# Kernel tuning notes

Measured on AMD Instinct MI355X. Metric: run time of the kernel, lower is better.

## Reference

```python
import jax, jax.numpy as jnp
import numpy as np

B, N, F = 32, 1024, 128
H = 256        # n_hidden and mlp_hidden widths
OUT = 3
BN_EPS = 1e-3  # keras BatchNormalization default epsilon


def setup_inputs() -> dict:
    key = jax.random.key(0)
    ks = jax.random.split(key, 16)
    x = jax.random.normal(ks[0], (B, N, F), dtype=jnp.float32)
    a = (jax.random.uniform(ks[1], (B, N, N)) < 0.02).astype(jnp.float32)
    eps = jnp.zeros((), dtype=jnp.float32)  # trainable GIN epsilon, init 0

    def dense_p(k, fi, fo):
        k1, k2 = jax.random.split(k)
        w = jax.random.normal(k1, (fi, fo), dtype=jnp.float32) * (1.0 / np.sqrt(fi))
        b = jnp.zeros((fo,), dtype=jnp.float32)
        return w, b

    def bn_p(k, f):
        k1, k2 = jax.random.split(k)
        g = 1.0 + 0.1 * jax.random.normal(k1, (f,), dtype=jnp.float32)
        be = 0.1 * jax.random.normal(k2, (f,), dtype=jnp.float32)
        m = 0.1 * jax.random.normal(jax.random.fold_in(k, 7), (f,), dtype=jnp.float32)
        v = jnp.ones((f,), dtype=jnp.float32)
        return g, be, m, v

    w1, b1 = dense_p(ks[2], F, H)
    g1, be1, m1, v1 = bn_p(ks[3], H)
    w2, b2 = dense_p(ks[4], H, H)
    g2, be2, m2, v2 = bn_p(ks[5], H)
    w3, b3 = dense_p(ks[6], H, H)   # final MLP dense -> n_hidden
    g3, be3, m3, v3 = bn_p(ks[7], H)
    wd, bd = dense_p(ks[8], H, OUT)
    return dict(x=x, a=a, eps=eps,
                w1=w1, b1=b1, g1=g1, be1=be1, m1=m1, v1=v1,
                w2=w2, b2=b2, g2=g2, be2=be2, m2=m2, v2=v2,
                w3=w3, b3=b3, g3=g3, be3=be3, m3=m3, v3=v3,
                wd=wd, bd=bd)


def _bn(h, g, be, m, v):
    # inference-mode batchnorm over last (feature) axis
    return (h - m) * (g / jnp.sqrt(v + BN_EPS)) + be


def reference(x, a, eps, w1, b1, g1, be1, m1, v1,
              w2, b2, g2, be2, m2, v2,
              w3, b3, g3, be3, m3, v3, wd, bd):
    # GIN aggregation: (1+eps)*x_i + sum_{j in N(i)} x_j
    agg = jnp.einsum('bij,bjf->bif', a, x)          # [B,N,F]
    h = (1.0 + eps) * x + agg
    # MLP: Dense->BN->relu x2 (mlp_hidden), then Dense(n_hidden)->BN->relu
    h = jax.nn.relu(_bn(h @ w1 + b1, g1, be1, m1, v1))  # [B,N,H]
    h = jax.nn.relu(_bn(h @ w2 + b2, g2, be2, m2, v2))
    h = jax.nn.relu(_bn(h @ w3 + b3, g3, be3, m3, v3))
    # global max pool over nodes, dropout(0) = identity, then head Dense(3)
    pooled = jnp.max(h, axis=1)                      # [B,H]
    return pooled @ wd + bd                          # [B,3]
```

## Files before the change

kernel.cpp:

```cpp
#include <hip/hip_runtime.h>

#define BN_EPS 1e-3f

typedef __attribute__((ext_vector_type(8))) short bf16x8;
typedef __attribute__((ext_vector_type(4))) float f32x4;

__device__ __forceinline__ short f2bf(float f) {
    union { float f; unsigned u; } a; a.f = f;
    unsigned r = a.u + 0x7fffu + ((a.u >> 16) & 1u);
    return (short)(r >> 16);
}
__device__ __forceinline__ float bf2f(short s) {
    union { unsigned u; float f; } a;
    a.u = ((unsigned)(unsigned short)s) << 16;
    return a.f;
}

__global__ __launch_bounds__(128) void agg_kernel(
    const float* __restrict__ x, const float* __restrict__ a,
    const float* __restrict__ epsp, float* __restrict__ h0) {
    const int row = blockIdx.x;
    const int b   = row >> 10;
    const int t   = threadIdx.x;

    __shared__ int idx[1024];
    __shared__ int cnt;
    if (t == 0) cnt = 0;
    __syncthreads();

    const float4* arow = reinterpret_cast<const float4*>(a + (size_t)row * 1024);
    float4 v0 = arow[t];
    float4 v1 = arow[t + 128];
    const int j0 = t * 4;
    if (v0.x != 0.f) idx[atomicAdd(&cnt, 1)] = j0 + 0;
    if (v0.y != 0.f) idx[atomicAdd(&cnt, 1)] = j0 + 1;
    if (v0.z != 0.f) idx[atomicAdd(&cnt, 1)] = j0 + 2;
    if (v0.w != 0.f) idx[atomicAdd(&cnt, 1)] = j0 + 3;
    if (v1.x != 0.f) idx[atomicAdd(&cnt, 1)] = 512 + j0 + 0;
    if (v1.y != 0.f) idx[atomicAdd(&cnt, 1)] = 512 + j0 + 1;
    if (v1.z != 0.f) idx[atomicAdd(&cnt, 1)] = 512 + j0 + 2;
    if (v1.w != 0.f) idx[atomicAdd(&cnt, 1)] = 512 + j0 + 3;
    __syncthreads();

    const int n = cnt;
    const float* xb = x + (size_t)b * (1024 * 128);
    float acc = (1.0f + epsp[0]) * xb[(size_t)(row & 1023) * 128 + t];
    for (int q = 0; q < n; ++q) {
        acc += xb[(size_t)idx[q] * 128 + t];
    }
    h0[(size_t)row * 128 + t] = acc;
}

__global__ __launch_bounds__(256) void prep_w(
    const float* __restrict__ w1, const float* __restrict__ w2,
    const float* __restrict__ w3, ushort* __restrict__ Wp) {
    const int k = blockIdx.x;
    const int c = threadIdx.x;
    const float* src; int kl, base;
    if (k < 128)      { src = w1; kl = k;       base = 0; }
    else if (k < 384) { src = w2; kl = k - 128; base = 65536; }
    else              { src = w3; kl = k - 384; base = 196608; }
    const float val = src[(size_t)kl * 256 + c];
    const short hi = f2bf(val);
    const short lo = f2bf(val - bf2f(hi));
    const int off = base + (kl >> 5) * 16384 + ((((kl >> 3) & 3) * 256 + c) * 8) + (kl & 7);
    Wp[off]        = (ushort)hi;
    Wp[off + 8192] = (ushort)lo;
}

__global__ __launch_bounds__(512, 2) void fused_mlp(
    const float* __restrict__ h0, const ushort* __restrict__ Wp,
    const float* __restrict__ b1, const float* __restrict__ g1,
    const float* __restrict__ be1, const float* __restrict__ m1,
    const float* __restrict__ v1,
    const float* __restrict__ b2, const float* __restrict__ g2,
    const float* __restrict__ be2, const float* __restrict__ m2,
    const float* __restrict__ v2,
    const float* __restrict__ b3, const float* __restrict__ g3,
    const float* __restrict__ be3, const float* __restrict__ m3,
    const float* __restrict__ v3,
    float* __restrict__ pool) {
    __shared__ __align__(16) ushort Wb[2][4][256][8];
    __shared__ __align__(16) ushort Ab[2][4][4][32][8];

    const int tid  = threadIdx.x;
    const int lane = tid & 63;
    const int wid  = tid >> 6;
    const int wr   = wid >> 1;
    const int wn   = wid & 1;
    const int lr   = lane & 15;
    const int kg   = lane >> 4;
    const int row0 = blockIdx.x * 128;

    f32x4 acc1[2][8] = {};
    f32x4 acc2[2][8] = {};

    const int arow = tid >> 2;
    const int akq  = tid & 3;
    const float* aptr = h0 + (size_t)(row0 + arow) * 128 + akq * 8;

    #pragma unroll
    for (int kc = 0; kc < 4; ++kc) {
        f32x4 a0 = *reinterpret_cast<const f32x4*>(aptr + kc * 32);
        f32x4 a1 = *reinterpret_cast<const f32x4*>(aptr + kc * 32 + 4);
        const f32x4* wsrc = reinterpret_cast<const f32x4*>(Wp + kc * 16384);
        f32x4 wv0 = wsrc[tid], wv1 = wsrc[512 + tid];
        f32x4 wv2 = wsrc[1024 + tid], wv3 = wsrc[1536 + tid];
        __syncthreads();
        {
            float av[8] = {a0.x, a0.y, a0.z, a0.w, a1.x, a1.y, a1.z, a1.w};
            bf16x8 hi, lo;
            #pragma unroll
            for (int e = 0; e < 8; ++e) {
                const short h = f2bf(av[e]);
                hi[e] = h; lo[e] = f2bf(av[e] - bf2f(h));
            }
            *reinterpret_cast<bf16x8*>(&Ab[0][arow >> 5][akq][arow & 31][0]) = hi;
            *reinterpret_cast<bf16x8*>(&Ab[1][arow >> 5][akq][arow & 31][0]) = lo;
        }
        f32x4* wdst = reinterpret_cast<f32x4*>(Wb);
        wdst[tid] = wv0; wdst[512 + tid] = wv1;
        wdst[1024 + tid] = wv2; wdst[1536 + tid] = wv3;
        __syncthreads();

        bf16x8 ah0 = *reinterpret_cast<bf16x8*>(&Ab[0][wr][kg][lr][0]);
        bf16x8 al0 = *reinterpret_cast<bf16x8*>(&Ab[1][wr][kg][lr][0]);
        bf16x8 ah1 = *reinterpret_cast<bf16x8*>(&Ab[0][wr][kg][16 + lr][0]);
        bf16x8 al1 = *reinterpret_cast<bf16x8*>(&Ab[1][wr][kg][16 + lr][0]);
        #pragma unroll
        for (int ni = 0; ni < 8; ++ni) {
            bf16x8 bh = *reinterpret_cast<bf16x8*>(&Wb[0][kg][wn * 128 + ni * 16 + lr][0]);
            bf16x8 bl = *reinterpret_cast<bf16x8*>(&Wb[1][kg][wn * 128 + ni * 16 + lr][0]);
            acc1[0][ni] = __builtin_amdgcn_mfma_f32_16x16x32_bf16(ah0, bh, acc1[0][ni], 0, 0, 0);
            acc1[0][ni] = __builtin_amdgcn_mfma_f32_16x16x32_bf16(ah0, bl, acc1[0][ni], 0, 0, 0);
            acc1[0][ni] = __builtin_amdgcn_mfma_f32_16x16x32_bf16(al0, bh, acc1[0][ni], 0, 0, 0);
            acc1[1][ni] = __builtin_amdgcn_mfma_f32_16x16x32_bf16(ah1, bh, acc1[1][ni], 0, 0, 0);
            acc1[1][ni] = __builtin_amdgcn_mfma_f32_16x16x32_bf16(ah1, bl, acc1[1][ni], 0, 0, 0);
            acc1[1][ni] = __builtin_amdgcn_mfma_f32_16x16x32_bf16(al1, bh, acc1[1][ni], 0, 0, 0);
        }
    }

    #pragma unroll
    for (int ni = 0; ni < 8; ++ni) {
        const int c = wn * 128 + ni * 16 + lr;
        const float s  = g1[c] * rsqrtf(v1[c] + BN_EPS);
        const float tt = be1[c] - m1[c] * s;
        const float bb = b1[c];
        #pragma unroll
        for (int mi = 0; mi < 2; ++mi)
            #pragma unroll
            for (int r = 0; r < 4; ++r)
                acc1[mi][ni][r] = fmaxf(fmaf(acc1[mi][ni][r] + bb, s, tt), 0.f);
    }

    #pragma unroll
    for (int kc = 0; kc < 8; ++kc) {
        const f32x4* wsrc = reinterpret_cast<const f32x4*>(Wp + 65536 + kc * 16384);
        f32x4 wv0 = wsrc[tid], wv1 = wsrc[512 + tid];
        f32x4 wv2 = wsrc[1024 + tid], wv3 = wsrc[1536 + tid];
        __syncthreads();
        if (wn == (kc >> 2)) {
            #pragma unroll
            for (int j = 0; j < 2; ++j) {
                const int ni  = (kc & 3) * 2 + j;
                const int kgw = j * 2 + (lr >> 3);
                const int e   = lr & 7;
                #pragma unroll
                for (int mi = 0; mi < 2; ++mi)
                    #pragma unroll
                    for (int r = 0; r < 4; ++r) {
                        const float val = acc1[mi][ni][r];
                        const short h = f2bf(val);
                        Ab[0][wr][kgw][mi * 16 + kg * 4 + r][e] = (ushort)h;
                        Ab[1][wr][kgw][mi * 16 + kg * 4 + r][e] = (ushort)f2bf(val - bf2f(h));
                    }
            }
        }
        f32x4* wdst = reinterpret_cast<f32x4*>(Wb);
        wdst[tid] = wv0; wdst[512 + tid] = wv1;
        wdst[1024 + tid] = wv2; wdst[1536 + tid] = wv3;
        __syncthreads();

        bf16x8 ah0 = *reinterpret_cast<bf16x8*>(&Ab[0][wr][kg][lr][0]);
        bf16x8 al0 = *reinterpret_cast<bf16x8*>(&Ab[1][wr][kg][lr][0]);
        bf16x8 ah1 = *reinterpret_cast<bf16x8*>(&Ab[0][wr][kg][16 + lr][0]);
        bf16x8 al1 = *reinterpret_cast<bf16x8*>(&Ab[1][wr][kg][16 + lr][0]);
        #pragma unroll
        for (int ni = 0; ni < 8; ++ni) {
            bf16x8 bh = *reinterpret_cast<bf16x8*>(&Wb[0][kg][wn * 128 + ni * 16 + lr][0]);
            bf16x8 bl = *reinterpret_cast<bf16x8*>(&Wb[1][kg][wn * 128 + ni * 16 + lr][0]);
            acc2[0][ni] = __builtin_amdgcn_mfma_f32_16x16x32_bf16(ah0, bh, acc2[0][ni], 0, 0, 0);
            acc2[0][ni] = __builtin_amdgcn_mfma_f32_16x16x32_bf16(ah0, bl, acc2[0][ni], 0, 0, 0);
            acc2[0][ni] = __builtin_amdgcn_mfma_f32_16x16x32_bf16(al0, bh, acc2[0][ni], 0, 0, 0);
            acc2[1][ni] = __builtin_amdgcn_mfma_f32_16x16x32_bf16(ah1, bh, acc2[1][ni], 0, 0, 0);
            acc2[1][ni] = __builtin_amdgcn_mfma_f32_16x16x32_bf16(ah1, bl, acc2[1][ni], 0, 0, 0);
            acc2[1][ni] = __builtin_amdgcn_mfma_f32_16x16x32_bf16(al1, bh, acc2[1][ni], 0, 0, 0);
        }
    }

    #pragma unroll
    for (int ni = 0; ni < 8; ++ni) {
        const int c = wn * 128 + ni * 16 + lr;
        const float s  = g2[c] * rsqrtf(v2[c] + BN_EPS);
        const float tt = be2[c] - m2[c] * s;
        const float bb = b2[c];
        #pragma unroll
        for (int mi = 0; mi < 2; ++mi)
            #pragma unroll
            for (int r = 0; r < 4; ++r)
                acc2[mi][ni][r] = fmaxf(fmaf(acc2[mi][ni][r] + bb, s, tt), 0.f);
    }

    #pragma unroll
    for (int mi = 0; mi < 2; ++mi)
        #pragma unroll
        for (int ni = 0; ni < 8; ++ni)
            #pragma unroll
            for (int r = 0; r < 4; ++r)
                acc1[mi][ni][r] = 0.f;

    #pragma unroll
    for (int kc = 0; kc < 8; ++kc) {
        const f32x4* wsrc = reinterpret_cast<const f32x4*>(Wp + 196608 + kc * 16384);
        f32x4 wv0 = wsrc[tid], wv1 = wsrc[512 + tid];
        f32x4 wv2 = wsrc[1024 + tid], wv3 = wsrc[1536 + tid];
        __syncthreads();
        if (wn == (kc >> 2)) {
            #pragma unroll
            for (int j = 0; j < 2; ++j) {
                const int ni  = (kc & 3) * 2 + j;
                const int kgw = j * 2 + (lr >> 3);
                const int e   = lr & 7;
                #pragma unroll
                for (int mi = 0; mi < 2; ++mi)
                    #pragma unroll
                    for (int r = 0; r < 4; ++r) {
                        const float val = acc2[mi][ni][r];
                        const short h = f2bf(val);
                        Ab[0][wr][kgw][mi * 16 + kg * 4 + r][e] = (ushort)h;
                        Ab[1][wr][kgw][mi * 16 + kg * 4 + r][e] = (ushort)f2bf(val - bf2f(h));
                    }
            }
        }
        f32x4* wdst = reinterpret_cast<f32x4*>(Wb);
        wdst[tid] = wv0; wdst[512 + tid] = wv1;
        wdst[1024 + tid] = wv2; wdst[1536 + tid] = wv3;
        __syncthreads();

        bf16x8 ah0 = *reinterpret_cast<bf16x8*>(&Ab[0][wr][kg][lr][0]);
        bf16x8 al0 = *reinterpret_cast<bf16x8*>(&Ab[1][wr][kg][lr][0]);
        bf16x8 ah1 = *reinterpret_cast<bf16x8*>(&Ab[0][wr][kg][16 + lr][0]);
        bf16x8 al1 = *reinterpret_cast<bf16x8*>(&Ab[1][wr][kg][16 + lr][0]);
        #pragma unroll
        for (int ni = 0; ni < 8; ++ni) {
            bf16x8 bh = *reinterpret_cast<bf16x8*>(&Wb[0][kg][wn * 128 + ni * 16 + lr][0]);
            bf16x8 bl = *reinterpret_cast<bf16x8*>(&Wb[1][kg][wn * 128 + ni * 16 + lr][0]);
            acc1[0][ni] = __builtin_amdgcn_mfma_f32_16x16x32_bf16(ah0, bh, acc1[0][ni], 0, 0, 0);
            acc1[0][ni] = __builtin_amdgcn_mfma_f32_16x16x32_bf16(ah0, bl, acc1[0][ni], 0, 0, 0);
            acc1[0][ni] = __builtin_amdgcn_mfma_f32_16x16x32_bf16(al0, bh, acc1[0][ni], 0, 0, 0);
            acc1[1][ni] = __builtin_amdgcn_mfma_f32_16x16x32_bf16(ah1, bh, acc1[1][ni], 0, 0, 0);
            acc1[1][ni] = __builtin_amdgcn_mfma_f32_16x16x32_bf16(ah1, bl, acc1[1][ni], 0, 0, 0);
            acc1[1][ni] = __builtin_amdgcn_mfma_f32_16x16x32_bf16(al1, bh, acc1[1][ni], 0, 0, 0);
        }
    }

    const int b = blockIdx.x >> 3;
    #pragma unroll
    for (int ni = 0; ni < 8; ++ni) {
        const int c = wn * 128 + ni * 16 + lr;
        const float s  = g3[c] * rsqrtf(v3[c] + BN_EPS);
        const float tt = be3[c] - m3[c] * s;
        const float bb = b3[c];
        float mx = 0.0f;
        #pragma unroll
        for (int mi = 0; mi < 2; ++mi)
            #pragma unroll
            for (int r = 0; r < 4; ++r)
                mx = fmaxf(mx, fmaf(acc1[mi][ni][r] + bb, s, tt));
        mx = fmaxf(mx, __shfl_xor(mx, 16));
        mx = fmaxf(mx, __shfl_xor(mx, 32));
        if (lane < 16)
            atomicMax((int*)&pool[b * 256 + c], __float_as_int(mx));
    }
}

__global__ __launch_bounds__(256) void pool_init(float* __restrict__ pool) {
    pool[blockIdx.x * 256 + threadIdx.x] = 0.0f;
}

__global__ __launch_bounds__(256) void head_kernel(const float* __restrict__ pool,
                                                   const float* __restrict__ wd,
                                                   const float* __restrict__ bd,
                                                   float* __restrict__ out) {
    const int b = blockIdx.x;
    const int t = threadIdx.x;
    const int w = t >> 6;
    const int lane = t & 63;
    if (w < 3) {
        float s = 0.f;
        #pragma unroll
        for (int k = 0; k < 256; k += 64)
            s += pool[b * 256 + k + lane] * wd[(k + lane) * 3 + w];
        #pragma unroll
        for (int off = 32; off; off >>= 1) s += __shfl_down(s, off);
        if (lane == 0) out[b * 3 + w] = s + bd[w];
    }
}

extern "C" void kernel_launch(void* const* d_in, const int* in_sizes, int n_in,
                              void* d_out, int out_size, void* d_ws, size_t ws_size,
                              hipStream_t stream) {
    const float* x   = (const float*)d_in[0];
    const float* a   = (const float*)d_in[1];
    const float* eps = (const float*)d_in[2];
    const float* w1  = (const float*)d_in[3];
    const float* b1  = (const float*)d_in[4];
    const float* g1  = (const float*)d_in[5];
    const float* be1 = (const float*)d_in[6];
    const float* m1  = (const float*)d_in[7];
    const float* v1  = (const float*)d_in[8];
    const float* w2  = (const float*)d_in[9];
    const float* b2  = (const float*)d_in[10];
    const float* g2  = (const float*)d_in[11];
    const float* be2 = (const float*)d_in[12];
    const float* m2  = (const float*)d_in[13];
    const float* v2  = (const float*)d_in[14];
    const float* w3  = (const float*)d_in[15];
    const float* b3  = (const float*)d_in[16];
    const float* g3  = (const float*)d_in[17];
    const float* be3 = (const float*)d_in[18];
    const float* m3  = (const float*)d_in[19];
    const float* v3  = (const float*)d_in[20];
    const float* wd  = (const float*)d_in[21];
    const float* bd  = (const float*)d_in[22];
    float* out = (float*)d_out;

    char* ws = (char*)d_ws;
    float*  h0   = (float*)(ws);
    ushort* Wp   = (ushort*)(ws + (16u << 20));
    float*  pool = (float*)(ws + (17u << 20));

    pool_init<<<32, 256, 0, stream>>>(pool);
    prep_w<<<640, 256, 0, stream>>>(w1, w2, w3, Wp);
    agg_kernel<<<32 * 1024, 128, 0, stream>>>(x, a, eps, h0);
    fused_mlp<<<256, 512, 0, stream>>>(h0, Wp,
        b1, g1, be1, m1, v1,
        b2, g2, be2, m2, v2,
        b3, g3, be3, m3, v3, pool);
    head_kernel<<<32, 256, 0, stream>>>(pool, wd, bd, out);
}
```

Before: 294.8 us.

## Replace sparse gather aggregation with dense bf16 MFMA GEMM over adjacency

```diff
diff --git a/kernel.cpp b/kernel.cpp
--- a/kernel.cpp
+++ b/kernel.cpp
@@ -16,39 +16,86 @@
     return a.f;
 }
 
-__global__ __launch_bounds__(128) void agg_kernel(
+__global__ __launch_bounds__(512, 2) void agg_mfma(
     const float* __restrict__ x, const float* __restrict__ a,
     const float* __restrict__ epsp, float* __restrict__ h0) {
-    const int row = blockIdx.x;
-    const int b   = row >> 10;
-    const int t   = threadIdx.x;
-
-    __shared__ int idx[1024];
-    __shared__ int cnt;
-    if (t == 0) cnt = 0;
-    __syncthreads();
-
-    const float4* arow = reinterpret_cast<const float4*>(a + (size_t)row * 1024);
-    float4 v0 = arow[t];
-    float4 v1 = arow[t + 128];
-    const int j0 = t * 4;
-    if (v0.x != 0.f) idx[atomicAdd(&cnt, 1)] = j0 + 0;
-    if (v0.y != 0.f) idx[atomicAdd(&cnt, 1)] = j0 + 1;
-    if (v0.z != 0.f) idx[atomicAdd(&cnt, 1)] = j0 + 2;
-    if (v0.w != 0.f) idx[atomicAdd(&cnt, 1)] = j0 + 3;
-    if (v1.x != 0.f) idx[atomicAdd(&cnt, 1)] = 512 + j0 + 0;
-    if (v1.y != 0.f) idx[atomicAdd(&cnt, 1)] = 512 + j0 + 1;
-    if (v1.z != 0.f) idx[atomicAdd(&cnt, 1)] = 512 + j0 + 2;
-    if (v1.w != 0.f) idx[atomicAdd(&cnt, 1)] = 512 + j0 + 3;
-    __syncthreads();
-
-    const int n = cnt;
-    const float* xb = x + (size_t)b * (1024 * 128);
-    float acc = (1.0f + epsp[0]) * xb[(size_t)(row & 1023) * 128 + t];
-    for (int q = 0; q < n; ++q) {
-        acc += xb[(size_t)idx[q] * 128 + t];
-    }
-    h0[(size_t)row * 128 + t] = acc;
+    __shared__ __align__(16) ushort Aab[4][128][8];
+    __shared__ __align__(16) ushort Xh[4][128][8];
+    __shared__ __align__(16) ushort Xl[4][128][8];
+
+    const int tid  = threadIdx.x;
+    const int lane = tid & 63;
+    const int wid  = tid >> 6;
+    const int wr   = wid >> 1;
+    const int wn   = wid & 1;
+    const int lr   = lane & 15;
+    const int kg   = lane >> 4;
+    const int b    = blockIdx.x >> 3;
+    const int row0 = (blockIdx.x & 7) * 128;
+
+    const float* ab = a + ((size_t)b * 1024 + row0) * 1024;
+    const float* xb = x + (size_t)b * 1024 * 128;
+
+    const int ai  = tid >> 2;
+    const int akq = tid & 3;
+    const int xkg = tid >> 7;
+    const int xf  = tid & 127;
+
+    f32x4 acc[2][4] = {};
+
+    for (int kc = 0; kc < 32; ++kc) {
+        const int k0 = kc * 32;
+        f32x4 a0 = *reinterpret_cast<const f32x4*>(ab + (size_t)ai * 1024 + k0 + akq * 8);
+        f32x4 a1 = *reinterpret_cast<const f32x4*>(ab + (size_t)ai * 1024 + k0 + akq * 8 + 4);
+        float xv[8];
+        #pragma unroll
+        for (int e = 0; e < 8; ++e)
+            xv[e] = xb[(size_t)(k0 + xkg * 8 + e) * 128 + xf];
+        __syncthreads();
+        {
+            float av[8] = {a0.x, a0.y, a0.z, a0.w, a1.x, a1.y, a1.z, a1.w};
+            bf16x8 h8;
+            #pragma unroll
+            for (int e = 0; e < 8; ++e) h8[e] = f2bf(av[e]);
+            *reinterpret_cast<bf16x8*>(&Aab[akq][ai][0]) = h8;
+            bf16x8 xh8, xl8;
+            #pragma unroll
+            for (int e = 0; e < 8; ++e) {
+                const short hh = f2bf(xv[e]);
+                xh8[e] = hh; xl8[e] = f2bf(xv[e] - bf2f(hh));
+            }
+            *reinterpret_cast<bf16x8*>(&Xh[xkg][xf][0]) = xh8;
+            *reinterpret_cast<bf16x8*>(&Xl[xkg][xf][0]) = xl8;
+        }
+        __syncthreads();
+
+        bf16x8 af0 = *reinterpret_cast<bf16x8*>(&Aab[kg][wr * 32 + lr][0]);
+        bf16x8 af1 = *reinterpret_cast<bf16x8*>(&Aab[kg][wr * 32 + 16 + lr][0]);
+        #pragma unroll
+        for (int ni = 0; ni < 4; ++ni) {
+            bf16x8 bh = *reinterpret_cast<bf16x8*>(&Xh[kg][wn * 64 + ni * 16 + lr][0]);
+            bf16x8 bl = *reinterpret_cast<bf16x8*>(&Xl[kg][wn * 64 + ni * 16 + lr][0]);
+            acc[0][ni] = __builtin_amdgcn_mfma_f32_16x16x32_bf16(af0, bh, acc[0][ni], 0, 0, 0);
+            acc[0][ni] = __builtin_amdgcn_mfma_f32_16x16x32_bf16(af0, bl, acc[0][ni], 0, 0, 0);
+            acc[1][ni] = __builtin_amdgcn_mfma_f32_16x16x32_bf16(af1, bh, acc[1][ni], 0, 0, 0);
+            acc[1][ni] = __builtin_amdgcn_mfma_f32_16x16x32_bf16(af1, bl, acc[1][ni], 0, 0, 0);
+        }
+    }
+
+    const float ep1 = 1.0f + epsp[0];
+    #pragma unroll
+    for (int ni = 0; ni < 4; ++ni) {
+        const int col = wn * 64 + ni * 16 + lr;
+        #pragma unroll
+        for (int mi = 0; mi < 2; ++mi) {
+            const int rbase = row0 + wr * 32 + mi * 16 + (lane >> 4) * 4;
+            #pragma unroll
+            for (int r = 0; r < 4; ++r) {
+                const size_t xoff = (size_t)(rbase + r) * 128 + col;
+                h0[(size_t)b * 131072 + xoff] = fmaf(ep1, xb[xoff], acc[mi][ni][r]);
+            }
+        }
+    }
 }
 
 __global__ __launch_bounds__(256) void prep_w(
@@ -342,7 +389,7 @@
 
     pool_init<<<32, 256, 0, stream>>>(pool);
     prep_w<<<640, 256, 0, stream>>>(w1, w2, w3, Wp);
-    agg_kernel<<<32 * 1024, 128, 0, stream>>>(x, a, eps, h0);
+    agg_mfma<<<256, 512, 0, stream>>>(x, a, eps, h0);
     fused_mlp<<<256, 512, 0, stream>>>(h0, Wp,
         b1, g1, be1, m1, v1,
         b2, g2, be2, m2, v2,
```

Result: slower. 313.4 us (+6.3%).

## Replace sparse gather aggregation with dense bf16 MFMA GEMM and shrink MLP tiles

Applied to the files above, without the earlier changes.

```diff
diff --git a/kernel.cpp b/kernel.cpp
--- a/kernel.cpp
+++ b/kernel.cpp
@@ -3,6 +3,7 @@
 #define BN_EPS 1e-3f
 
 typedef __attribute__((ext_vector_type(8))) short bf16x8;
+typedef __attribute__((ext_vector_type(4))) short short4v;
 typedef __attribute__((ext_vector_type(4))) float f32x4;
 
 __device__ __forceinline__ short f2bf(float f) {
@@ -16,39 +17,88 @@
     return a.f;
 }
 
-__global__ __launch_bounds__(128) void agg_kernel(
+__global__ __launch_bounds__(512) void prep_x(const float* __restrict__ x,
+                                              ushort* __restrict__ Xp) {
+    const int b  = blockIdx.x >> 5;
+    const int kc = blockIdx.x & 31;
+    const int t  = threadIdx.x;
+    const int f  = t & 127;
+    const int kg = t >> 7;
+    bf16x8 hi8, lo8;
+    #pragma unroll
+    for (int e = 0; e < 8; ++e) {
+        const float val = x[((size_t)b * 1024 + kc * 32 + kg * 8 + e) * 128 + f];
+        const short h = f2bf(val);
+        hi8[e] = h; lo8[e] = f2bf(val - bf2f(h));
+    }
+    const size_t base = ((size_t)(b * 32 + kc)) * 8192 + (size_t)kg * 1024 + (size_t)f * 8;
+    *reinterpret_cast<bf16x8*>(&Xp[base])        = hi8;
+    *reinterpret_cast<bf16x8*>(&Xp[base + 4096]) = lo8;
+}
+
+__global__ __launch_bounds__(512, 4) void agg_mfma(
     const float* __restrict__ x, const float* __restrict__ a,
-    const float* __restrict__ epsp, float* __restrict__ h0) {
-    const int row = blockIdx.x;
-    const int b   = row >> 10;
-    const int t   = threadIdx.x;
-
-    __shared__ int idx[1024];
-    __shared__ int cnt;
-    if (t == 0) cnt = 0;
-    __syncthreads();
-
-    const float4* arow = reinterpret_cast<const float4*>(a + (size_t)row * 1024);
-    float4 v0 = arow[t];
-    float4 v1 = arow[t + 128];
-    const int j0 = t * 4;
-    if (v0.x != 0.f) idx[atomicAdd(&cnt, 1)] = j0 + 0;
-    if (v0.y != 0.f) idx[atomicAdd(&cnt, 1)] = j0 + 1;
-    if (v0.z != 0.f) idx[atomicAdd(&cnt, 1)] = j0 + 2;
-    if (v0.w != 0.f) idx[atomicAdd(&cnt, 1)] = j0 + 3;
-    if (v1.x != 0.f) idx[atomicAdd(&cnt, 1)] = 512 + j0 + 0;
-    if (v1.y != 0.f) idx[atomicAdd(&cnt, 1)] = 512 + j0 + 1;
-    if (v1.z != 0.f) idx[atomicAdd(&cnt, 1)] = 512 + j0 + 2;
-    if (v1.w != 0.f) idx[atomicAdd(&cnt, 1)] = 512 + j0 + 3;
-    __syncthreads();
-
-    const int n = cnt;
-    const float* xb = x + (size_t)b * (1024 * 128);
-    float acc = (1.0f + epsp[0]) * xb[(size_t)(row & 1023) * 128 + t];
-    for (int q = 0; q < n; ++q) {
-        acc += xb[(size_t)idx[q] * 128 + t];
-    }
-    h0[(size_t)row * 128 + t] = acc;
+    const ushort* __restrict__ Xp, const float* __restrict__ epsp,
+    float* __restrict__ h0) {
+    __shared__ __align__(16) ushort Aab[4][64][8];
+    __shared__ __align__(16) ushort Xhl[2][4][128][8];
+
+    const int tid  = threadIdx.x;
+    const int lane = tid & 63;
+    const int wid  = tid >> 6;
+    const int wr   = wid >> 1;
+    const int wn   = wid & 1;
+    const int lr   = lane & 15;
+    const int kg   = lane >> 4;
+    const int b    = blockIdx.x >> 4;
+    const int row0 = (blockIdx.x & 15) * 64;
+
+    const float*  ab = a + ((size_t)b * 1024 + row0) * 1024;
+    const ushort* xp = Xp + (size_t)b * 32 * 8192;
+
+    const int ai  = tid >> 3;
+    const int akq = tid & 7;
+
+    f32x4 acc[4] = {};
+
+    for (int kc = 0; kc < 32; ++kc) {
+        f32x4 av = *reinterpret_cast<const f32x4*>(ab + (size_t)ai * 1024 + kc * 32 + akq * 4);
+        const f32x4* xsrc = reinterpret_cast<const f32x4*>(xp + (size_t)kc * 8192);
+        f32x4 xv0 = xsrc[tid];
+        f32x4 xv1 = xsrc[512 + tid];
+        __syncthreads();
+        {
+            short4v h4;
+            h4[0] = f2bf(av.x); h4[1] = f2bf(av.y);
+            h4[2] = f2bf(av.z); h4[3] = f2bf(av.w);
+            *reinterpret_cast<short4v*>(&Aab[akq >> 1][ai][(akq & 1) * 4]) = h4;
+        }
+        f32x4* xdst = reinterpret_cast<f32x4*>(Xhl);
+        xdst[tid] = xv0; xdst[512 + tid] = xv1;
+        __syncthreads();
+
+        bf16x8 af = *reinterpret_cast<bf16x8*>(&Aab[kg][wr * 16 + lr][0]);
+        #pragma unroll
+        for (int ni = 0; ni < 4; ++ni) {
+            bf16x8 bh = *reinterpret_cast<bf16x8*>(&Xhl[0][kg][wn * 64 + ni * 16 + lr][0]);
+            bf16x8 bl = *reinterpret_cast<bf16x8*>(&Xhl[1][kg][wn * 64 + ni * 16 + lr][0]);
+            acc[ni] = __builtin_amdgcn_mfma_f32_16x16x32_bf16(af, bh, acc[ni], 0, 0, 0);
+            acc[ni] = __builtin_amdgcn_mfma_f32_16x16x32_bf16(af, bl, acc[ni], 0, 0, 0);
+        }
+    }
+
+    const float ep1 = 1.0f + epsp[0];
+    const float* xb = x + (size_t)b * 131072;
+    #pragma unroll
+    for (int ni = 0; ni < 4; ++ni) {
+        const int col   = wn * 64 + ni * 16 + lr;
+        const int rbase = row0 + wr * 16 + kg * 4;
+        #pragma unroll
+        for (int r = 0; r < 4; ++r) {
+            const size_t off = (size_t)(rbase + r) * 128 + col;
+            h0[(size_t)b * 131072 + off] = fmaf(ep1, xb[off], acc[ni][r]);
+        }
+    }
 }
 
 __global__ __launch_bounds__(256) void prep_w(
@@ -68,7 +118,7 @@
     Wp[off + 8192] = (ushort)lo;
 }
 
-__global__ __launch_bounds__(512, 2) void fused_mlp(
+__global__ __launch_bounds__(512, 4) void fused_mlp(
     const float* __restrict__ h0, const ushort* __restrict__ Wp,
     const float* __restrict__ b1, const float* __restrict__ g1,
     const float* __restrict__ be1, const float* __restrict__ m1,
@@ -81,42 +131,41 @@
     const float* __restrict__ v3,
     float* __restrict__ pool) {
     __shared__ __align__(16) ushort Wb[2][4][256][8];
-    __shared__ __align__(16) ushort Ab[2][4][4][32][8];
+    __shared__ __align__(16) ushort Ab[2][2][4][32][8];
 
     const int tid  = threadIdx.x;
     const int lane = tid & 63;
     const int wid  = tid >> 6;
-    const int wr   = wid >> 1;
-    const int wn   = wid & 1;
+    const int wr   = wid >> 2;
+    const int wn   = wid & 3;
     const int lr   = lane & 15;
     const int kg   = lane >> 4;
-    const int row0 = blockIdx.x * 128;
-
-    f32x4 acc1[2][8] = {};
-    f32x4 acc2[2][8] = {};
-
-    const int arow = tid >> 2;
-    const int akq  = tid & 3;
-    const float* aptr = h0 + (size_t)(row0 + arow) * 128 + akq * 8;
+    const int row0 = blockIdx.x * 64;
+
+    f32x4 acc1[2][4] = {};
+    f32x4 acc2[2][4] = {};
+
+    const int arow = tid >> 3;
+    const int akq  = tid & 7;
+    const float* aptr = h0 + (size_t)(row0 + arow) * 128 + akq * 4;
 
     #pragma unroll
     for (int kc = 0; kc < 4; ++kc) {
-        f32x4 a0 = *reinterpret_cast<const f32x4*>(aptr + kc * 32);
-        f32x4 a1 = *reinterpret_cast<const f32x4*>(aptr + kc * 32 + 4);
+        f32x4 av = *reinterpret_cast<const f32x4*>(aptr + kc * 32);
         const f32x4* wsrc = reinterpret_cast<const f32x4*>(Wp + kc * 16384);
         f32x4 wv0 = wsrc[tid], wv1 = wsrc[512 + tid];
         f32x4 wv2 = wsrc[1024 + tid], wv3 = wsrc[1536 + tid];
         __syncthreads();
         {
-            float av[8] = {a0.x, a0.y, a0.z, a0.w, a1.x, a1.y, a1.z, a1.w};
-            bf16x8 hi, lo;
-            #pragma unroll
-            for (int e = 0; e < 8; ++e) {
-                const short h = f2bf(av[e]);
-                hi[e] = h; lo[e] = f2bf(av[e] - bf2f(h));
+            float fx[4] = {av.x, av.y, av.z, av.w};
+            short4v h4, l4;
+            #pragma unroll
+            for (int e = 0; e < 4; ++e) {
+                const short h = f2bf(fx[e]);
+                h4[e] = h; l4[e] = f2bf(fx[e] - bf2f(h));
             }
-            *reinterpret_cast<bf16x8*>(&Ab[0][arow >> 5][akq][arow & 31][0]) = hi;
-            *reinterpret_cast<bf16x8*>(&Ab[1][arow >> 5][akq][arow & 31][0]) = lo;
+            *reinterpret_cast<short4v*>(&Ab[0][arow >> 5][akq >> 1][arow & 31][(akq & 1) * 4]) = h4;
+            *reinterpret_cast<short4v*>(&Ab[1][arow >> 5][akq >> 1][arow & 31][(akq & 1) * 4]) = l4;
         }
         f32x4* wdst = reinterpret_cast<f32x4*>(Wb);
         wdst[tid] = wv0; wdst[512 + tid] = wv1;
@@ -128,9 +177,9 @@
         bf16x8 ah1 = *reinterpret_cast<bf16x8*>(&Ab[0][wr][kg][16 + lr][0]);
         bf16x8 al1 = *reinterpret_cast<bf16x8*>(&Ab[1][wr][kg][16 + lr][0]);
         #pragma unroll
-        for (int ni = 0; ni < 8; ++ni) {
-            bf16x8 bh = *reinterpret_cast<bf16x8*>(&Wb[0][kg][wn * 128 + ni * 16 + lr][0]);
-            bf16x8 bl = *reinterpret_cast<bf16x8*>(&Wb[1][kg][wn * 128 + ni * 16 + lr][0]);
+        for (int ni = 0; ni < 4; ++ni) {
+            bf16x8 bh = *reinterpret_cast<bf16x8*>(&Wb[0][kg][wn * 64 + ni * 16 + lr][0]);
+            bf16x8 bl = *reinterpret_cast<bf16x8*>(&Wb[1][kg][wn * 64 + ni * 16 + lr][0]);
             acc1[0][ni] = __builtin_amdgcn_mfma_f32_16x16x32_bf16(ah0, bh, acc1[0][ni], 0, 0, 0);
             acc1[0][ni] = __builtin_amdgcn_mfma_f32_16x16x32_bf16(ah0, bl, acc1[0][ni], 0, 0, 0);
             acc1[0][ni] = __builtin_amdgcn_mfma_f32_16x16x32_bf16(al0, bh, acc1[0][ni], 0, 0, 0);
@@ -141,8 +190,8 @@
     }
 
     #pragma unroll
-    for (int ni = 0; ni < 8; ++ni) {
-        const int c = wn * 128 + ni * 16 + lr;
+    for (int ni = 0; ni < 4; ++ni) {
+        const int c = wn * 64 + ni * 16 + lr;
         const float s  = g1[c] * rsqrtf(v1[c] + BN_EPS);
         const float tt = be1[c] - m1[c] * s;
         const float bb = b1[c];
@@ -159,10 +208,10 @@
         f32x4 wv0 = wsrc[tid], wv1 = wsrc[512 + tid];
         f32x4 wv2 = wsrc[1024 + tid], wv3 = wsrc[1536 + tid];
         __syncthreads();
-        if (wn == (kc >> 2)) {
+        if (wn == (kc >> 1)) {
             #pragma unroll
             for (int j = 0; j < 2; ++j) {
-                const int ni  = (kc & 3) * 2 + j;
+                const int ni  = (kc & 1) * 2 + j;
                 const int kgw = j * 2 + (lr >> 3);
                 const int e   = lr & 7;
                 #pragma unroll
@@ -186,9 +235,9 @@
         bf16x8 ah1 = *reinterpret_cast<bf16x8*>(&Ab[0][wr][kg][16 + lr][0]);
         bf16x8 al1 = *reinterpret_cast<bf16x8*>(&Ab[1][wr][kg][16 + lr][0]);
         #pragma unroll
-        for (int ni = 0; ni < 8; ++ni) {
-            bf16x8 bh = *reinterpret_cast<bf16x8*>(&Wb[0][kg][wn * 128 + ni * 16 + lr][0]);
-            bf16x8 bl = *reinterpret_cast<bf16x8*>(&Wb[1][kg][wn * 128 + ni * 16 + lr][0]);
+        for (int ni = 0; ni < 4; ++ni) {
+            bf16x8 bh = *reinterpret_cast<bf16x8*>(&Wb[0][kg][wn * 64 + ni * 16 + lr][0]);
+            bf16x8 bl = *reinterpret_cast<bf16x8*>(&Wb[1][kg][wn * 64 + ni * 16 + lr][0]);
             acc2[0][ni] = __builtin_amdgcn_mfma_f32_16x16x32_bf16(ah0, bh, acc2[0][ni], 0, 0, 0);
             acc2[0][ni] = __builtin_amdgcn_mfma_f32_16x16x32_bf16(ah0, bl, acc2[0][ni], 0, 0, 0);
             acc2[0][ni] = __builtin_amdgcn_mfma_f32_16x16x32_bf16(al0, bh, acc2[0][ni], 0, 0, 0);
@@ -199,8 +248,8 @@
     }
 
     #pragma unroll
-    for (int ni = 0; ni < 8; ++ni) {
-        const int c = wn * 128 + ni * 16 + lr;
+    for (int ni = 0; ni < 4; ++ni) {
+        const int c = wn * 64 + ni * 16 + lr;
         const float s  = g2[c] * rsqrtf(v2[c] + BN_EPS);
         const float tt = be2[c] - m2[c] * s;
         const float bb = b2[c];
@@ -214,7 +263,7 @@
     #pragma unroll
     for (int mi = 0; mi < 2; ++mi)
         #pragma unroll
-        for (int ni = 0; ni < 8; ++ni)
+        for (int ni = 0; ni < 4; ++ni)
             #pragma unroll
             for (int r = 0; r < 4; ++r)
                 acc1[mi][ni][r] = 0.f;
@@ -225,10 +274,10 @@
         f32x4 wv0 = wsrc[tid], wv1 = wsrc[512 + tid];
         f32x4 wv2 = wsrc[1024 + tid], wv3 = wsrc[1536 + tid];
         __syncthreads();
-        if (wn == (kc >> 2)) {
+        if (wn == (kc >> 1)) {
             #pragma unroll
             for (int j = 0; j < 2; ++j) {
-                const int ni  = (kc & 3) * 2 + j;
+                const int ni  = (kc & 1) * 2 + j;
                 const int kgw = j * 2 + (lr >> 3);
                 const int e   = lr & 7;
                 #pragma unroll
@@ -252,9 +301,9 @@
         bf16x8 ah1 = *reinterpret_cast<bf16x8*>(&Ab[0][wr][kg][16 + lr][0]);
         bf16x8 al1 = *reinterpret_cast<bf16x8*>(&Ab[1][wr][kg][16 + lr][0]);
         #pragma unroll
-        for (int ni = 0; ni < 8; ++ni) {
-            bf16x8 bh = *reinterpret_cast<bf16x8*>(&Wb[0][kg][wn * 128 + ni * 16 + lr][0]);
-            bf16x8 bl = *reinterpret_cast<bf16x8*>(&Wb[1][kg][wn * 128 + ni * 16 + lr][0]);
+        for (int ni = 0; ni < 4; ++ni) {
+            bf16x8 bh = *reinterpret_cast<bf16x8*>(&Wb[0][kg][wn * 64 + ni * 16 + lr][0]);
+            bf16x8 bl = *reinterpret_cast<bf16x8*>(&Wb[1][kg][wn * 64 + ni * 16 + lr][0]);
             acc1[0][ni] = __builtin_amdgcn_mfma_f32_16x16x32_bf16(ah0, bh, acc1[0][ni], 0, 0, 0);
             acc1[0][ni] = __builtin_amdgcn_mfma_f32_16x16x32_bf16(ah0, bl, acc1[0][ni], 0, 0, 0);
             acc1[0][ni] = __builtin_amdgcn_mfma_f32_16x16x32_bf16(al0, bh, acc1[0][ni], 0, 0, 0);
@@ -264,10 +313,10 @@
         }
     }
 
-    const int b = blockIdx.x >> 3;
-    #pragma unroll
-    for (int ni = 0; ni < 8; ++ni) {
-        const int c = wn * 128 + ni * 16 + lr;
+    const int b = blockIdx.x >> 4;
+    #pragma unroll
+    for (int ni = 0; ni < 4; ++ni) {
+        const int c = wn * 64 + ni * 16 + lr;
         const float s  = g3[c] * rsqrtf(v3[c] + BN_EPS);
         const float tt = be3[c] - m3[c] * s;
         const float bb = b3[c];
@@ -338,12 +387,14 @@
     char* ws = (char*)d_ws;
     float*  h0   = (float*)(ws);
     ushort* Wp   = (ushort*)(ws + (16u << 20));
-    float*  pool = (float*)(ws + (17u << 20));
+    ushort* Xp   = (ushort*)(ws + (18u << 20));
+    float*  pool = (float*)(ws + (34u << 20));
 
     pool_init<<<32, 256, 0, stream>>>(pool);
     prep_w<<<640, 256, 0, stream>>>(w1, w2, w3, Wp);
-    agg_kernel<<<32 * 1024, 128, 0, stream>>>(x, a, eps, h0);
-    fused_mlp<<<256, 512, 0, stream>>>(h0, Wp,
+    prep_x<<<1024, 512, 0, stream>>>(x, Xp);
+    agg_mfma<<<512, 512, 0, stream>>>(x, a, Xp, eps, h0);
+    fused_mlp<<<512, 512, 0, stream>>>(h0, Wp,
         b1, g1, be1, m1, v1,
         b2, g2, be2, m2, v2,
         b3, g3, be3, m3, v3, pool);
```

Result: slower. 316.0 us (+7.2%).
